# Performance work log

Hardware: AMD Instinct MI355X
Metric: run time of the kernel (lower is better)

The kernel has to match this reference:

```python
import jax, jax.numpy as jnp
import numpy as np

B, G, N_IN, N_HID, N_OUT = 2, 4096, 8, 32, 32
ALPHA, BETA, BN_EPS = 0.005, 5e-5, 1e-5
EDGE_P = 0.05  # adjacency density


def _lin_init(k, fan_in, fan_out):
    k1, k2 = jax.random.split(k)
    lim = 1.0 / np.sqrt(fan_in)
    W = jax.random.uniform(k1, (fan_in, fan_out), minval=-lim, maxval=lim, dtype=jnp.float32)
    b = jax.random.uniform(k2, (fan_out,), minval=-lim, maxval=lim, dtype=jnp.float32)
    return W, b


def setup_inputs() -> dict:
    key = jax.random.key(0)
    ks = jax.random.split(key, 12)
    W_infer, b_infer = _lin_init(ks[0], N_IN, N_HID)
    W_e1, b_e1 = _lin_init(ks[1], 2 * N_HID, 1)
    W_e2, b_e2 = _lin_init(ks[2], 2 * N_HID, 1)
    W_n1, b_n1 = _lin_init(ks[3], 2 * N_HID, N_OUT)
    W_n2, b_n2 = _lin_init(ks[4], 2 * N_HID, N_OUT)
    W_m1, b_m1 = _lin_init(ks[5], 2 * N_HID, N_OUT)
    W_m2, b_m2 = _lin_init(ks[6], 2 * N_HID, N_OUT)
    x = jax.random.normal(ks[7], (B, G, N_IN), dtype=jnp.float32)
    edges1 = jax.random.bernoulli(ks[8], EDGE_P, (G, G)).astype(jnp.float32)
    edges2 = jax.random.bernoulli(ks[9], EDGE_P, (G, G)).astype(jnp.float32)
    bn_gamma = jnp.ones((G,), jnp.float32)
    bn_beta = jnp.zeros((G,), jnp.float32)
    return dict(x=x, edges1=edges1, edges2=edges2, W_infer=W_infer, b_infer=b_infer,
                W_e1=W_e1, b_e1=b_e1, W_e2=W_e2, b_e2=b_e2,
                W_n1=W_n1, b_n1=b_n1, W_n2=W_n2, b_n2=b_n2,
                W_m1=W_m1, b_m1=b_m1, W_m2=W_m2, b_m2=b_m2,
                bn_gamma=bn_gamma, bn_beta=bn_beta)


def _mp_block(x, adj, coef, W_e, b_e, W_n, b_n, W_m, b_m):
    # x: [B,G,H]. Torch builds edge feature at flat index k=i*G+j as cat([x_j, x_i])
    # (shape2 = col gather, shape1 = row gather). We keep the same math without
    # materializing the [B,G*G,2H] tensor.
    Hh = x.shape[-1]
    s_src = x @ W_e[:Hh]   # [B,G,1]  (x_j part of mlp_edge)
    s_dst = x @ W_e[Hh:]   # [B,G,1]  (x_i part of mlp_edge)
    logits = s_dst[:, :, None, 0] + s_src[:, None, :, 0] + b_e[0]   # [B,G,G] at (i,j)
    w = adj + coef * (adj == 0).astype(x.dtype)                     # ori_edge + coef*thres_edge
    e = jax.nn.sigmoid(logits) * w[None]                            # [B,G,G]
    # receive at node i: sum_j e_ij * [x_j, x_i]
    recv_src = jnp.einsum('bij,bjh->bih', e, x)                     # sum_j e_ij x_j
    recv_dst = x * jnp.sum(e, axis=2)[..., None]                    # x_i * sum_j e_ij
    recv = jnp.concatenate([recv_src, recv_dst], axis=-1)           # [B,G,2H]
    recv = jax.nn.elu(recv @ W_n + b_n)                             # nodes_mlp + elu
    upd = jnp.concatenate([recv, x], axis=-1) @ W_m + b_m           # mesg_merge (mode='cat')
    return jax.nn.elu(upd)


def _forward(x, edges1, edges2, W_infer, b_infer, W_e1, b_e1, W_e2, b_e2,
             W_n1, b_n1, W_n2, b_n2, W_m1, b_m1, W_m2, b_m2, bn_gamma, bn_beta):
    h = jax.nn.elu(x @ W_infer + b_infer)                           # infer + elu, [B,G,H]
    h = _mp_block(h, edges1, ALPHA, W_e1, b_e1, W_n1, b_n1, W_m1, b_m1)
    # BatchNorm1d(gene_num) on [B, G, n_out]: per-gene stats over (batch, feature)
    mu = jnp.mean(h, axis=(0, 2), keepdims=True)
    var = jnp.var(h, axis=(0, 2), keepdims=True)
    h = (h - mu) * jax.lax.rsqrt(var + BN_EPS)
    h = h * bn_gamma[None, :, None] + bn_beta[None, :, None]
    return _mp_block(h, edges2, BETA, W_e2, b_e2, W_n2, b_n2, W_m2, b_m2)


def reference(x, edges1, edges2, W_infer, b_infer, W_e1, b_e1, W_e2, b_e2,
              W_n1, b_n1, W_n2, b_n2, W_m1, b_m1, W_m2, b_m2, bn_gamma, bn_beta):
    return _forward(x, edges1, edges2, W_infer, b_infer, W_e1, b_e1, W_e2, b_e2,
                    W_n1, b_n1, W_n2, b_n2, W_m1, b_m1, W_m2, b_m2, bn_gamma, bn_beta)
```

## Files before the change

kernel.cpp:

```cpp
#include <hip/hip_runtime.h>

#define G 4096
#define BSZ 2
#define NIN 8
#define HID 32
#define JSN 8
#define CHUNK 512

typedef __attribute__((ext_vector_type(8))) short short8;
typedef __attribute__((ext_vector_type(4))) float floatx4;
typedef __attribute__((ext_vector_type(4))) short short4v;
typedef unsigned short ushort_t;

__device__ __forceinline__ float elu1(float v) {
    return v > 0.f ? v : (__expf(v) - 1.f);
}
__device__ __forceinline__ ushort_t f2bf(float f) {
    unsigned u = __float_as_uint(f);
    u += 0x7fffu + ((u >> 16) & 1u);
    return (ushort_t)(u >> 16);
}

__global__ __launch_bounds__(256) void k_setup1(
    const float* __restrict__ x, const float* __restrict__ W,
    const float* __restrict__ bias, const float* __restrict__ We,
    float* __restrict__ h0, ushort_t* __restrict__ hTb,
    float* __restrict__ ssrc, float* __restrict__ sdst) {
    __shared__ __align__(16) ushort_t hs[HID][264];
    int tid = threadIdx.x;
    int t = blockIdx.x * 256 + tid;
    int b = t >> 12;
    int g0 = (blockIdx.x & 15) * 256;
    float xin[NIN];
    const float* xp = x + t * NIN;
#pragma unroll
    for (int k = 0; k < NIN; k++) xin[k] = xp[k];
    float ss = 0.f, sd = 0.f;
    float* hp = h0 + (size_t)t * HID;
#pragma unroll
    for (int o = 0; o < HID; o++) {
        float v = bias[o];
#pragma unroll
        for (int k = 0; k < NIN; k++) v += xin[k] * W[k * HID + o];
        v = elu1(v);
        hp[o] = v;
        hs[o][tid] = f2bf(v);
        ss += v * We[o];
        sd += v * We[HID + o];
    }
    ssrc[t] = ss;
    sdst[t] = sd;
    __syncthreads();
#pragma unroll
    for (int p = 0; p < 4; p++) {
        int row = p * 8 + (tid >> 5);
        int c = (tid & 31) * 8;
        short8 v8 = *(const short8*)&hs[row][c];
        *(short8*)(void*)&hTb[(size_t)(b * HID + row) * G + g0 + c] = v8;
    }
}

__global__ __launch_bounds__(512, 8) void k_main(
    const float* __restrict__ adj, const float* __restrict__ ssrc,
    const float* __restrict__ sdst, const ushort_t* __restrict__ hTb,
    const float* __restrict__ bep, float coef,
    float* __restrict__ part_recv, float* __restrict__ part_es) {
    __shared__ __align__(16) float ssm[BSZ][CHUNK];
    __shared__ float red[4][64][9];
    int tid = threadIdx.x;
    int w = tid >> 6, l = tid & 63;
    int b = w >> 2, ihalf = (w >> 1) & 1, jh = w & 1;
    int i0 = blockIdx.x * 32;
    int jbase = blockIdx.y * CHUNK;
    if (tid < 256) {
        int bb = tid >> 7, ix = (tid & 127) * 4;
        *(float4*)&ssm[bb][ix] = *(const float4*)&ssrc[bb * G + jbase + ix];
    }
    int m = l & 15, kg = l >> 4;
    int i = i0 + ihalf * 16 + m;
    float sd = sdst[b * G + i] + bep[0];
    float wm1 = 1.f - coef;
    int joff = jbase + jh * 256 + kg * 8;
    const float* adjrow = adj + (size_t)i * G + joff;
    const ushort_t* hb0 = hTb + (size_t)(b * HID + m) * G + joff;
    const ushort_t* hb1 = hb0 + (size_t)16 * G;
    floatx4 c0 = {0.f, 0.f, 0.f, 0.f}, c1 = {0.f, 0.f, 0.f, 0.f};
    float es = 0.f;

    float4 pa0[2], pa1[2];
    short8 pb0[2], pb1[2];
#pragma unroll
    for (int d = 0; d < 2; d++) {
        pa0[d] = *(const float4*)(adjrow + d * 32);
        pa1[d] = *(const float4*)(adjrow + d * 32 + 4);
        pb0[d] = *(const short8*)(const void*)(hb0 + d * 32);
        pb1[d] = *(const short8*)(const void*)(hb1 + d * 32);
    }
    __syncthreads();
    const float* svp = &ssm[b][jh * 256 + kg * 8];

#pragma unroll
    for (int jc = 0; jc < 8; jc++) {
        int cur = jc & 1;
        float4 a0 = pa0[cur], a1 = pa1[cur];
        short8 bf0 = pb0[cur], bf1 = pb1[cur];
        if (jc + 2 < 8) {
            int o = (jc + 2) * 32;
            pa0[cur] = *(const float4*)(adjrow + o);
            pa1[cur] = *(const float4*)(adjrow + o + 4);
            pb0[cur] = *(const short8*)(const void*)(hb0 + o);
            pb1[cur] = *(const short8*)(const void*)(hb1 + o);
        }
        float4 s0 = *(const float4*)&svp[jc * 32];
        float4 s1 = *(const float4*)&svp[jc * 32 + 4];
        float av[8] = {a0.x, a0.y, a0.z, a0.w, a1.x, a1.y, a1.z, a1.w};
        float sv[8] = {s0.x, s0.y, s0.z, s0.w, s1.x, s1.y, s1.z, s1.w};
        short8 af;
#pragma unroll
        for (int t = 0; t < 8; t++) {
            float wgt = __builtin_fmaf(av[t], wm1, coef);
            float sg = __builtin_amdgcn_rcpf(1.f + __expf(-(sd + sv[t])));
            float e = sg * wgt;
            es += e;
            af[t] = (short)f2bf(e);
        }
        c0 = __builtin_amdgcn_mfma_f32_16x16x32_bf16(af, bf0, c0, 0, 0, 0);
        c1 = __builtin_amdgcn_mfma_f32_16x16x32_bf16(af, bf1, c1, 0, 0, 0);
    }
    int slot = w >> 1;
    if (jh) {
#pragma unroll
        for (int r = 0; r < 4; r++) {
            red[slot][l][r] = c0[r];
            red[slot][l][4 + r] = c1[r];
        }
        red[slot][l][8] = es;
    }
    __syncthreads();
    if (!jh) {
#pragma unroll
        for (int r = 0; r < 4; r++) {
            c0[r] += red[slot][l][r];
            c1[r] += red[slot][l][4 + r];
        }
        es += red[slot][l][8];
        es += __shfl_xor(es, 16);
        es += __shfl_xor(es, 32);
        size_t rb = ((size_t)(blockIdx.y * BSZ + b)) * G;
#pragma unroll
        for (int r = 0; r < 4; r++) {
            int row = i0 + ihalf * 16 + kg * 4 + r;
            part_recv[(rb + row) * 32 + m] = c0[r];
            part_recv[(rb + row) * 32 + 16 + m] = c1[r];
        }
        if (l < 16) part_es[rb + i] = es;
    }
}

template <bool DO_BN>
__global__ __launch_bounds__(256) void k_post(
    const float* __restrict__ part_recv, const float* __restrict__ part_es,
    const float* __restrict__ hin,
    const float* __restrict__ Wn, const float* __restrict__ bnb,
    const float* __restrict__ Wm, const float* __restrict__ bmb,
    const float* __restrict__ gamma, const float* __restrict__ beta,
    const float* __restrict__ We2, float* __restrict__ outp,
    ushort_t* __restrict__ hTb, float* __restrict__ s2s,
    float* __restrict__ s2d) {
    __shared__ float Wns[64 * 32];
    __shared__ float Wms[64 * 32];
    __shared__ float rec[8][68];
    __shared__ float rec2[8][68];
    __shared__ ushort_t tb[BSZ][HID][4];
    int tid = threadIdx.x;
    int rl = tid >> 5, hh = tid & 31;
#pragma unroll
    for (int r = 0; r < 8; r++) {
        Wns[r * 256 + tid] = Wn[r * 256 + tid];
        Wms[r * 256 + tid] = Wm[r * 256 + tid];
    }
    int g0 = blockIdx.x * 4;
    int b = rl & 1;
    int g = g0 + (rl >> 1);
    int rowf = b * G + g;
    float rs = 0.f, es = 0.f;
#pragma unroll
    for (int js = 0; js < JSN; js++) {
        size_t sb = (size_t)(js * BSZ + b) * G + g;
        rs += part_recv[sb * 32 + hh];
        es += part_es[sb];
    }
    float xv = hin[(size_t)rowf * HID + hh];
    rec[rl][hh] = rs;
    rec[rl][32 + hh] = xv * es;
    __syncthreads();
    float v = bnb[hh];
#pragma unroll
    for (int k4 = 0; k4 < 16; k4++) {
        float4 r4 = *(const float4*)&rec[rl][k4 * 4];
        v += r4.x * Wns[(k4 * 4 + 0) * HID + hh];
        v += r4.y * Wns[(k4 * 4 + 1) * HID + hh];
        v += r4.z * Wns[(k4 * 4 + 2) * HID + hh];
        v += r4.w * Wns[(k4 * 4 + 3) * HID + hh];
    }
    v = elu1(v);
    rec2[rl][hh] = v;
    rec2[rl][32 + hh] = xv;
    __syncthreads();
    float u = bmb[hh];
#pragma unroll
    for (int k4 = 0; k4 < 16; k4++) {
        float4 r4 = *(const float4*)&rec2[rl][k4 * 4];
        u += r4.x * Wms[(k4 * 4 + 0) * HID + hh];
        u += r4.y * Wms[(k4 * 4 + 1) * HID + hh];
        u += r4.z * Wms[(k4 * 4 + 2) * HID + hh];
        u += r4.w * Wms[(k4 * 4 + 3) * HID + hh];
    }
    float h1v = elu1(u);
    if (!DO_BN) {
        outp[(size_t)rowf * HID + hh] = h1v;
    } else {
        float s = h1v, sq = h1v * h1v;
#pragma unroll
        for (int mm = 32; mm; mm >>= 1) {
            s += __shfl_xor(s, mm);
            sq += __shfl_xor(sq, mm);
        }
        float mu = s * (1.f / 64.f);
        float var = sq * (1.f / 64.f) - mu * mu;
        float rstd = rsqrtf(var + 1e-5f);
        float hn = (h1v - mu) * rstd * gamma[g] + beta[g];
        outp[(size_t)rowf * HID + hh] = hn;
        tb[b][hh][rl >> 1] = f2bf(hn);
        float ps = hn * We2[hh], pd = hn * We2[HID + hh];
#pragma unroll
        for (int mm = 16; mm; mm >>= 1) {
            ps += __shfl_xor(ps, mm);
            pd += __shfl_xor(pd, mm);
        }
        if (hh == 0) {
            s2s[rowf] = ps;
            s2d[rowf] = pd;
        }
        __syncthreads();
        if (tid < 64) {
            int b2 = tid >> 5, c = tid & 31;
            short4v val = *(const short4v*)&tb[b2][c][0];
            *(short4v*)(void*)&hTb[(size_t)(b2 * HID + c) * G + g0] = val;
        }
    }
}

extern "C" void kernel_launch(void* const* d_in, const int* in_sizes, int n_in,
                              void* d_out, int out_size, void* d_ws, size_t ws_size,
                              hipStream_t stream) {
    const float* x      = (const float*)d_in[0];
    const float* edges1 = (const float*)d_in[1];
    const float* edges2 = (const float*)d_in[2];
    const float* W_inf  = (const float*)d_in[3];
    const float* b_inf  = (const float*)d_in[4];
    const float* W_e1   = (const float*)d_in[5];
    const float* b_e1   = (const float*)d_in[6];
    const float* W_e2   = (const float*)d_in[7];
    const float* b_e2   = (const float*)d_in[8];
    const float* W_n1   = (const float*)d_in[9];
    const float* b_n1   = (const float*)d_in[10];
    const float* W_n2   = (const float*)d_in[11];
    const float* b_n2   = (const float*)d_in[12];
    const float* W_m1   = (const float*)d_in[13];
    const float* b_m1   = (const float*)d_in[14];
    const float* W_m2   = (const float*)d_in[15];
    const float* b_m2   = (const float*)d_in[16];
    const float* bn_g   = (const float*)d_in[17];
    const float* bn_b   = (const float*)d_in[18];
    float* out = (float*)d_out;

    float* ws = (float*)d_ws;
    float* h0   = ws;
    float* h1n  = ws + 262144;
    float* s1s  = ws + 524288;
    float* s1d  = ws + 532480;
    float* s2s  = ws + 540672;
    float* s2d  = ws + 548864;
    float* part_recv = ws + 557056;
    float* part_es   = ws + 2654208;
    ushort_t* hTb = (ushort_t*)(ws + 2719744);

    const float ALPHA = 0.005f, BETA = 5e-5f;

    k_setup1<<<32, 256, 0, stream>>>(x, W_inf, b_inf, W_e1, h0, hTb, s1s, s1d);
    k_main<<<dim3(G / 32, JSN), 512, 0, stream>>>(edges1, s1s, s1d, hTb, b_e1, ALPHA,
                                                  part_recv, part_es);
    k_post<true><<<G / 4, 256, 0, stream>>>(part_recv, part_es, h0, W_n1, b_n1,
                                            W_m1, b_m1, bn_g, bn_b, W_e2, h1n,
                                            hTb, s2s, s2d);
    k_main<<<dim3(G / 32, JSN), 512, 0, stream>>>(edges2, s2s, s2d, hTb, b_e2, BETA,
                                                  part_recv, part_es);
    k_post<false><<<G / 4, 256, 0, stream>>>(part_recv, part_es, h1n, W_n2, b_n2,
                                             W_m2, b_m2, nullptr, nullptr, nullptr,
                                             out, nullptr, nullptr, nullptr);
}
```

Baseline: 240.8 us.

## Pack adjacency matrices into bitmasks and use exp2-based sigmoid in main kernel

Adds a pre-pass kernel that turns both float adjacency matrices into 1-bit masks via wave ballots. The main message-passing kernels then read those bits through shared memory instead of streaming 64 MB of float adjacency each, which takes global-load and register pressure off the MFMA loop. The sigmoid also switches to exp2 with the -log2(e) factor applied in advance to the source and destination scores. Total DRAM reads of the adjacency stay about the same, since the pack pass still reads both matrices once; the gain has to come from a cheaper, better-coalesced streaming pass and a lighter main loop.

```diff
diff --git a/kernel.cpp b/kernel.cpp
--- a/kernel.cpp
+++ b/kernel.cpp
@@ -6,11 +6,14 @@
 #define HID 32
 #define JSN 8
 #define CHUNK 512
+#define NLOG2E (-1.4426950408889634f)
 
 typedef __attribute__((ext_vector_type(8))) short short8;
 typedef __attribute__((ext_vector_type(4))) float floatx4;
 typedef __attribute__((ext_vector_type(4))) short short4v;
 typedef unsigned short ushort_t;
+typedef unsigned int uint_t;
+typedef unsigned long long u64_t;
 
 __device__ __forceinline__ float elu1(float v) {
     return v > 0.f ? v : (__expf(v) - 1.f);
@@ -19,6 +22,30 @@
     unsigned u = __float_as_uint(f);
     u += 0x7fffu + ((u >> 16) & 1u);
     return (ushort_t)(u >> 16);
+}
+
+__global__ __launch_bounds__(256) void k_pack(
+    const float* __restrict__ e1, const float* __restrict__ e2,
+    uint_t* __restrict__ pk) {
+    int wid = blockIdx.x * 4 + (threadIdx.x >> 6);
+    int lane = threadIdx.x & 63;
+    int matrix = wid >> 11;
+    int ul = (wid & 2047) * 128;
+    const float* src = matrix ? e2 : e1;
+    u64_t* dst = (u64_t*)(pk + (size_t)matrix * 524288);
+    for (int s = 0; s < 128; s += 8) {
+        float v[8];
+#pragma unroll
+        for (int k = 0; k < 8; k++)
+            v[k] = src[(size_t)(ul + s + k) * 64 + lane];
+        u64_t mk[8];
+#pragma unroll
+        for (int k = 0; k < 8; k++) mk[k] = __ballot(v[k] != 0.f);
+        if (lane == 0) {
+#pragma unroll
+            for (int k = 0; k < 8; k++) dst[ul + s + k] = mk[k];
+        }
+    }
 }
 
 __global__ __launch_bounds__(256) void k_setup1(
@@ -61,11 +88,12 @@
 }
 
 __global__ __launch_bounds__(512, 8) void k_main(
-    const float* __restrict__ adj, const float* __restrict__ ssrc,
+    const uint_t* __restrict__ pk, const float* __restrict__ ssrc,
     const float* __restrict__ sdst, const ushort_t* __restrict__ hTb,
     const float* __restrict__ bep, float coef,
     float* __restrict__ part_recv, float* __restrict__ part_es) {
     __shared__ __align__(16) float ssm[BSZ][CHUNK];
+    __shared__ uint_t abits[32 * 17];
     __shared__ float red[4][64][9];
     int tid = threadIdx.x;
     int w = tid >> 6, l = tid & 63;
@@ -74,53 +102,54 @@
     int jbase = blockIdx.y * CHUNK;
     if (tid < 256) {
         int bb = tid >> 7, ix = (tid & 127) * 4;
-        *(float4*)&ssm[bb][ix] = *(const float4*)&ssrc[bb * G + jbase + ix];
+        float4 s4 = *(const float4*)&ssrc[bb * G + jbase + ix];
+        s4.x *= NLOG2E; s4.y *= NLOG2E; s4.z *= NLOG2E; s4.w *= NLOG2E;
+        *(float4*)&ssm[bb][ix] = s4;
+    }
+    {
+        int r = tid >> 4, d = tid & 15;
+        abits[r * 17 + d] = pk[(size_t)(i0 + r) * 128 + blockIdx.y * 16 + d];
     }
     int m = l & 15, kg = l >> 4;
     int i = i0 + ihalf * 16 + m;
-    float sd = sdst[b * G + i] + bep[0];
+    float sd2 = (sdst[b * G + i] + bep[0]) * NLOG2E;
     float wm1 = 1.f - coef;
     int joff = jbase + jh * 256 + kg * 8;
-    const float* adjrow = adj + (size_t)i * G + joff;
     const ushort_t* hb0 = hTb + (size_t)(b * HID + m) * G + joff;
     const ushort_t* hb1 = hb0 + (size_t)16 * G;
     floatx4 c0 = {0.f, 0.f, 0.f, 0.f}, c1 = {0.f, 0.f, 0.f, 0.f};
     float es = 0.f;
 
-    float4 pa0[2], pa1[2];
     short8 pb0[2], pb1[2];
 #pragma unroll
     for (int d = 0; d < 2; d++) {
-        pa0[d] = *(const float4*)(adjrow + d * 32);
-        pa1[d] = *(const float4*)(adjrow + d * 32 + 4);
         pb0[d] = *(const short8*)(const void*)(hb0 + d * 32);
         pb1[d] = *(const short8*)(const void*)(hb1 + d * 32);
     }
     __syncthreads();
     const float* svp = &ssm[b][jh * 256 + kg * 8];
+    const uint_t* abp = &abits[(ihalf * 16 + m) * 17 + jh * 8];
 
 #pragma unroll
     for (int jc = 0; jc < 8; jc++) {
         int cur = jc & 1;
-        float4 a0 = pa0[cur], a1 = pa1[cur];
         short8 bf0 = pb0[cur], bf1 = pb1[cur];
         if (jc + 2 < 8) {
             int o = (jc + 2) * 32;
-            pa0[cur] = *(const float4*)(adjrow + o);
-            pa1[cur] = *(const float4*)(adjrow + o + 4);
             pb0[cur] = *(const short8*)(const void*)(hb0 + o);
             pb1[cur] = *(const short8*)(const void*)(hb1 + o);
         }
+        uint_t bw = abp[jc];
         float4 s0 = *(const float4*)&svp[jc * 32];
         float4 s1 = *(const float4*)&svp[jc * 32 + 4];
-        float av[8] = {a0.x, a0.y, a0.z, a0.w, a1.x, a1.y, a1.z, a1.w};
         float sv[8] = {s0.x, s0.y, s0.z, s0.w, s1.x, s1.y, s1.z, s1.w};
         short8 af;
 #pragma unroll
         for (int t = 0; t < 8; t++) {
-            float wgt = __builtin_fmaf(av[t], wm1, coef);
-            float sg = __builtin_amdgcn_rcpf(1.f + __expf(-(sd + sv[t])));
-            float e = sg * wgt;
+            float bitf = (float)((bw >> (kg * 8 + t)) & 1u);
+            float wgt = __builtin_fmaf(bitf, wm1, coef);
+            float ex = exp2f(sd2 + sv[t]);
+            float e = __builtin_amdgcn_rcpf(1.f + ex) * wgt;
             es += e;
             af[t] = (short)f2bf(e);
         }
@@ -285,17 +314,19 @@
     float* part_recv = ws + 557056;
     float* part_es   = ws + 2654208;
     ushort_t* hTb = (ushort_t*)(ws + 2719744);
+    uint_t* pk = (uint_t*)(ws + 2850816);
 
     const float ALPHA = 0.005f, BETA = 5e-5f;
 
+    k_pack<<<1024, 256, 0, stream>>>(edges1, edges2, pk);
     k_setup1<<<32, 256, 0, stream>>>(x, W_inf, b_inf, W_e1, h0, hTb, s1s, s1d);
-    k_main<<<dim3(G / 32, JSN), 512, 0, stream>>>(edges1, s1s, s1d, hTb, b_e1, ALPHA,
+    k_main<<<dim3(G / 32, JSN), 512, 0, stream>>>(pk, s1s, s1d, hTb, b_e1, ALPHA,
                                                   part_recv, part_es);
     k_post<true><<<G / 4, 256, 0, stream>>>(part_recv, part_es, h0, W_n1, b_n1,
                                             W_m1, b_m1, bn_g, bn_b, W_e2, h1n,
                                             hTb, s2s, s2d);
-    k_main<<<dim3(G / 32, JSN), 512, 0, stream>>>(edges2, s2s, s2d, hTb, b_e2, BETA,
-                                                  part_recv, part_es);
+    k_main<<<dim3(G / 32, JSN), 512, 0, stream>>>(pk + 524288, s2s, s2d, hTb, b_e2,
+                                                  BETA, part_recv, part_es);
     k_post<false><<<G / 4, 256, 0, stream>>>(part_recv, part_es, h1n, W_n2, b_n2,
                                              W_m2, b_m2, nullptr, nullptr, nullptr,
                                              out, nullptr, nullptr, nullptr);
```

Result: slower. 293.5 us (+21.9%).
